# Kernel tuning notes

Measured on AMD Instinct MI355X. Metric: run time of the kernel, lower is better.

Reference implementation:

```python
import jax, jax.numpy as jnp
import numpy as np

N_NODES = 100000
N_EDGES = 3200000
IN_F = 128


def gcn_conv(x, edge_index, edge_weight, W, b):
    """PyG GCNConv: add self-loops (weight 1), symmetric normalization,
    scatter-add aggregation from src -> dst, then bias."""
    n = x.shape[0]
    src, dst = edge_index[0], edge_index[1]
    h = x @ W  # [N, out]
    # degree with self-loop weight 1
    deg = jax.ops.segment_sum(edge_weight, dst, num_segments=n) + 1.0
    dinv = jax.lax.rsqrt(deg)
    norm = dinv[src] * edge_weight * dinv[dst]  # [E]
    msgs = norm[:, None] * h[src]  # [E, out]
    out = jax.ops.segment_sum(msgs, dst, num_segments=n)
    # self-loop contribution: norm = dinv*1*dinv = 1/deg
    out = out + h / deg[:, None]
    return out + b


def setup_inputs() -> dict:
    key = jax.random.key(0)
    ks = jax.random.split(key, 12)
    x = jax.random.normal(ks[0], (N_NODES, IN_F), dtype=jnp.float32)
    edge_index = jax.random.randint(ks[1], (2, N_EDGES), 0, N_NODES)
    edge_weights = jax.random.uniform(ks[2], (N_EDGES,), dtype=jnp.float32)
    def glorot(k, shape):
        lim = np.sqrt(6.0 / (shape[0] + shape[1]))
        return jax.random.uniform(k, shape, jnp.float32, -lim, lim)
    return {
        "x": x,
        "edge_index": edge_index,
        "edge_weights": edge_weights,
        "W1": glorot(ks[3], (IN_F, 32)),
        "b1": jnp.zeros((32,), jnp.float32),
        "W2": glorot(ks[4], (32, 16)),
        "b2": jnp.zeros((16,), jnp.float32),
        "fc1_w": glorot(ks[5], (16, 1)),
        "fc1_b": jnp.zeros((1,), jnp.float32),
        "fc2_w": glorot(ks[6], (33, 1)),
        "fc2_b": jnp.zeros((1,), jnp.float32),
    }


def reference(x, edge_index, edge_weights, W1, b1, W2, b2, fc1_w, fc1_b, fc2_w, fc2_b):
    x1 = gcn_conv(x, edge_index, edge_weights, W1, b1)
    h = jax.nn.relu(x1)  # dropout is identity in eval mode
    x2 = gcn_conv(h, edge_index, edge_weights, W2, b2)
    x1f = x2 @ fc1_w + fc1_b        # [N, 1]
    c = jax.nn.sigmoid(x1f)
    cat = jnp.concatenate([h, c], axis=1)  # [N, 33]
    r = cat @ fc2_w + fc2_b         # [N, 1]
    return (r, x1f)
```

## Files before the change

kernel.cpp:

```cpp
#include <hip/hip_runtime.h>
#include <math.h>


#define TPB 256
#define PA_CHUNK 4096
#define KMAXB 512
#define NPW 8

__global__ __launch_bounds__(512) void countA_kernel(const int* __restrict__ dst,
                                                     int* __restrict__ gtot,
                                                     int E, int K) {
    __shared__ int lhist[KMAXB];
    const int tid = threadIdx.x;
    const int e0  = blockIdx.x * PA_CHUNK;
    if (tid < KMAXB) lhist[tid] = 0;
    __syncthreads();
#pragma unroll
    for (int i = 0; i < 8; ++i) {
        int e = e0 + tid + i * 512;
        if (e < E) atomicAdd(&lhist[dst[e] >> 8], 1);
    }
    __syncthreads();
    if (tid < K && lhist[tid] > 0) atomicAdd(&gtot[tid], lhist[tid]);
}

__global__ __launch_bounds__(64) void kscan_kernel(const int* __restrict__ gtot,
                                                   int* __restrict__ gstart,
                                                   int* __restrict__ gcursor,
                                                   int K, int E) {
    int tid = threadIdx.x;
    int b0 = tid * 8, v[8], s = 0;
#pragma unroll
    for (int t = 0; t < 8; ++t) {
        v[t] = s;
        int idx = b0 + t;
        s += (idx < K) ? gtot[idx] : 0;
    }
    int incl = s;
#pragma unroll
    for (int d = 1; d < 64; d <<= 1) {
        int t2 = __shfl_up(incl, d);
        if (tid >= d) incl += t2;
    }
    int excl = incl - s;
#pragma unroll
    for (int t = 0; t < 8; ++t) {
        int idx = b0 + t;
        if (idx < K) { gstart[idx] = excl + v[t]; gcursor[idx] = excl + v[t]; }
    }
    if (tid == 63) gstart[K] = E;
}

__global__ __launch_bounds__(512) void placeA_kernel(const int* __restrict__ src,
                                                     const int* __restrict__ dst,
                                                     const float* __restrict__ ew,
                                                     uint2* __restrict__ tmp,
                                                     int* __restrict__ gcursor,
                                                     int E, int K) {
    __shared__ int lhist[KMAXB], lbase[KMAXB], lcur[KMAXB], gbaseS[KMAXB];
    __shared__ int ltot;
    __shared__ uint2 stage[PA_CHUNK];
    __shared__ int   saddr[PA_CHUNK];
    const int tid = threadIdx.x;
    const int e0  = blockIdx.x * PA_CHUNK;

    if (tid < KMAXB) { lhist[tid] = 0; lcur[tid] = 0; }
    __syncthreads();

    int   b[8];
    uint2 p[8];
#pragma unroll
    for (int i = 0; i < 8; ++i) {
        int e = e0 + tid + i * 512;
        b[i] = -1;
        if (e < E) {
            int d   = dst[e];
            int s   = src[e];
            float w = ew[e];
            b[i]   = d >> 8;
            p[i].x = __float_as_uint(w);
            p[i].y = ((unsigned)s << 8) | (unsigned)(d & 255);
            atomicAdd(&lhist[b[i]], 1);
        }
    }
    __syncthreads();

    if (tid < 64) {
        int b0 = tid * 8, v[8], s = 0;
#pragma unroll
        for (int t = 0; t < 8; ++t) { v[t] = s; s += lhist[b0 + t]; }
        int incl = s;
#pragma unroll
        for (int d = 1; d < 64; d <<= 1) {
            int t2 = __shfl_up(incl, d);
            if (tid >= d) incl += t2;
        }
        int excl = incl - s;
#pragma unroll
        for (int t = 0; t < 8; ++t) lbase[b0 + t] = excl + v[t];
        if (tid == 63) ltot = incl;
    }
    __syncthreads();

    if (tid < K && lhist[tid] > 0)
        gbaseS[tid] = atomicAdd(&gcursor[tid], lhist[tid]);
    __syncthreads();

#pragma unroll
    for (int i = 0; i < 8; ++i) {
        if (b[i] >= 0) {
            int r    = atomicAdd(&lcur[b[i]], 1);
            int sidx = lbase[b[i]] + r;
            stage[sidx] = p[i];
            saddr[sidx] = gbaseS[b[i]] + r;
        }
    }
    __syncthreads();

    int tot = ltot;
    for (int s = tid; s < tot; s += 512) tmp[saddr[s]] = stage[s];
}

__global__ __launch_bounds__(512) void partB_kernel(const uint2* __restrict__ tmp,
                                                    const int* __restrict__ gstart,
                                                    int2* __restrict__ epair,
                                                    int* __restrict__ off,
                                                    float* __restrict__ dinv,
                                                    int N) {
    __shared__ int   lhist[256], loff[256], lcur[256];
    __shared__ float ldeg[256];
    const int tid  = threadIdx.x;
    const int k    = blockIdx.x;
    const int seg0 = gstart[k], seg1 = gstart[k + 1];

    if (tid < 256) { lhist[tid] = 0; lcur[tid] = 0; ldeg[tid] = 0.f; }
    __syncthreads();

    for (int j = seg0 + tid; j < seg1; j += 512)
        atomicAdd(&lhist[tmp[j].y & 255u], 1);
    __syncthreads();

    if (tid < 64) {
        int b0 = tid * 4, v[4], s = 0;
#pragma unroll
        for (int t = 0; t < 4; ++t) { v[t] = s; s += lhist[b0 + t]; }
        int incl = s;
#pragma unroll
        for (int d = 1; d < 64; d <<= 1) {
            int t2 = __shfl_up(incl, d);
            if (tid >= d) incl += t2;
        }
        int excl = incl - s;
#pragma unroll
        for (int t = 0; t < 4; ++t) loff[b0 + t] = excl + v[t];
    }
    __syncthreads();

    if (tid < 256) {
        int d = (k << 8) + tid;
        if (d < N) off[d] = seg0 + loff[tid];
    }

    for (int j = seg0 + tid; j < seg1; j += 512) {
        uint2 q  = tmp[j];
        int dlow = q.y & 255u;
        int s    = (int)(q.y >> 8);
        float w  = __uint_as_float(q.x);
        int r    = atomicAdd(&lcur[dlow], 1);
        int2 pr; pr.x = s; pr.y = (int)q.x;
        epair[seg0 + loff[dlow] + r] = pr;
        atomicAdd(&ldeg[dlow], w);
    }
    __syncthreads();

    if (tid < 256) {
        int d = (k << 8) + tid;
        if (d < N) dinv[d] = 1.0f / sqrtf(ldeg[tid] + 1.0f);
    }
}

__global__ __launch_bounds__(TPB) void gemm1_kernel(const float* __restrict__ x,
                                                    const float* __restrict__ W,
                                                    const float* __restrict__ dinv,
                                                    float* __restrict__ h, int N) {
    __shared__ float Ws[128 * 32];
    __shared__ float xs[32 * 129];
    const int tid = threadIdx.x;
    const int nb  = blockIdx.x * 32;

    const float4* W4  = (const float4*)W;
    float4*       Ws4 = (float4*)Ws;
#pragma unroll
    for (int i = 0; i < 4; ++i) Ws4[tid + i * 256] = W4[tid + i * 256];

#pragma unroll
    for (int i = 0; i < 4; ++i) {
        int idx  = tid + i * 256;
        int node = idx >> 5;
        int col4 = idx & 31;
        if (nb + node < N) {
            float4 v = ((const float4*)(x + (size_t)nb * 128))[idx];
            float* p = &xs[node * 129 + col4 * 4];
            p[0] = v.x; p[1] = v.y; p[2] = v.z; p[3] = v.w;
        }
    }
    __syncthreads();

    const int nl = tid >> 3;
    const int og = (tid & 7) * 4;
    float a0 = 0.f, a1 = 0.f, a2 = 0.f, a3 = 0.f;
#pragma unroll 8
    for (int k = 0; k < 128; ++k) {
        float xv = xs[nl * 129 + k];
        const float* wp = &Ws[k * 32 + og];
        a0 = fmaf(xv, wp[0], a0);
        a1 = fmaf(xv, wp[1], a1);
        a2 = fmaf(xv, wp[2], a2);
        a3 = fmaf(xv, wp[3], a3);
    }
    int node = nb + nl;
    if (node < N) {
        float dv = dinv[node];
        float* out = &h[(size_t)node * 32 + og];
        out[0] = a0 * dv; out[1] = a1 * dv; out[2] = a2 * dv; out[3] = a3 * dv;
    }
}

__global__ __launch_bounds__(TPB) void gather32_fused_kernel(
    const int* __restrict__ off, const int2* __restrict__ epair,
    const float* __restrict__ g1, const float* __restrict__ dinv,
    const float* __restrict__ b1, const float* __restrict__ W2,
    const float* __restrict__ fc2_w,
    float* __restrict__ g2, float* __restrict__ rdot, int N, int E) {
    __shared__ float wls[544];
    const int tid = threadIdx.x;
    wls[tid]       = W2[tid];
    wls[tid + 256] = W2[tid + 256];
    if (tid < 32) wls[512 + tid] = fc2_w[tid];
    __syncthreads();

    const int lane = tid & 63;
    const int f    = lane & 31;
    const int half = lane >> 5;
    const float bv = b1[f];
    const int wbase = (lane < 16) ? lane : 512;
    const int wstrd = (lane < 16) ? 16 : 1;

    const int i0 = (blockIdx.x * (TPB / 64) + (tid >> 6)) * NPW;

    for (int t = 0; t < NPW; ++t) {
        int i = i0 + t;
        if (i >= N) return;
        const int s0 = off[i];
        const int s1 = (i + 1 < N) ? off[i + 1] : E;

        float acc = 0.f;
        int j = s0 + half;
        for (; j + 6 < s1; j += 8) {
            int2 pa = epair[j];
            int2 pb = epair[j + 2];
            int2 pc = epair[j + 4];
            int2 pd = epair[j + 6];
            acc = fmaf(__int_as_float(pa.y), g1[(size_t)pa.x * 32 + f], acc);
            acc = fmaf(__int_as_float(pb.y), g1[(size_t)pb.x * 32 + f], acc);
            acc = fmaf(__int_as_float(pc.y), g1[(size_t)pc.x * 32 + f], acc);
            acc = fmaf(__int_as_float(pd.y), g1[(size_t)pd.x * 32 + f], acc);
        }
        for (; j < s1; j += 2) {
            int2 p = epair[j];
            acc = fmaf(__int_as_float(p.y), g1[(size_t)p.x * 32 + f], acc);
        }
        acc += __shfl_xor(acc, 32);

        float dv = dinv[i];
        float v  = fmaxf(dv * (acc + g1[(size_t)i * 32 + f]) + bv, 0.f);

        float hs = 0.f;
#pragma unroll
        for (int k = 0; k < 32; ++k)
            hs = fmaf(__shfl(v, k), wls[wbase + k * wstrd], hs);

        if (lane < 16)       g2[(size_t)i * 16 + lane] = hs * dv;
        else if (lane == 16) rdot[i] = hs;
    }
}

__global__ __launch_bounds__(TPB) void gather16_final_kernel(
    const int* __restrict__ off, const int2* __restrict__ epair,
    const float* __restrict__ g2, const float* __restrict__ rdot,
    const float* __restrict__ dinv, const float* __restrict__ b2,
    const float* __restrict__ fc1_w, const float* __restrict__ fc1_b,
    const float* __restrict__ fc2_w, const float* __restrict__ fc2_b,
    float* __restrict__ out, int N, int E) {
    const int tid  = threadIdx.x;
    const int lane = tid & 63;
    const int f    = lane & 15;
    const int q    = lane >> 4;
    const float b2v = b2[f];
    const float f1v = fc1_w[f];
    const float f1b = fc1_b[0];
    const float f2w = fc2_w[32];
    const float f2b = fc2_b[0];

    const int i0 = (blockIdx.x * (TPB / 64) + (tid >> 6)) * NPW;

    for (int t = 0; t < NPW; ++t) {
        int i = i0 + t;
        if (i >= N) return;
        const int s0 = off[i];
        const int s1 = (i + 1 < N) ? off[i + 1] : E;

        float acc = 0.f;
        int j = s0 + q;
        for (; j + 12 < s1; j += 16) {
            int2 pa = epair[j];
            int2 pb = epair[j + 4];
            int2 pc = epair[j + 8];
            int2 pd = epair[j + 12];
            acc = fmaf(__int_as_float(pa.y), g2[(size_t)pa.x * 16 + f], acc);
            acc = fmaf(__int_as_float(pb.y), g2[(size_t)pb.x * 16 + f], acc);
            acc = fmaf(__int_as_float(pc.y), g2[(size_t)pc.x * 16 + f], acc);
            acc = fmaf(__int_as_float(pd.y), g2[(size_t)pd.x * 16 + f], acc);
        }
        for (; j < s1; j += 4) {
            int2 p = epair[j];
            acc = fmaf(__int_as_float(p.y), g2[(size_t)p.x * 16 + f], acc);
        }
        acc += __shfl_xor(acc, 16);
        acc += __shfl_xor(acc, 32);

        float dv = dinv[i];
        float x2 = dv * (acc + g2[(size_t)i * 16 + f]) + b2v;

        float part = x2 * f1v;
        part += __shfl_xor(part, 1);
        part += __shfl_xor(part, 2);
        part += __shfl_xor(part, 4);
        part += __shfl_xor(part, 8);
        float x1f = part + f1b;
        float c   = 1.0f / (1.0f + expf(-x1f));
        float r   = fmaf(c, f2w, f2b) + rdot[i];

        if (lane == 0) {
            out[i]     = r;
            out[N + i] = x1f;
        }
    }
}

extern "C" void kernel_launch(void* const* d_in, const int* in_sizes, int n_in,
                              void* d_out, int out_size, void* d_ws, size_t ws_size,
                              hipStream_t stream) {
    const float* x     = (const float*)d_in[0];
    const int*   ei    = (const int*)d_in[1];
    const float* ew    = (const float*)d_in[2];
    const float* W1    = (const float*)d_in[3];
    const float* b1    = (const float*)d_in[4];
    const float* W2    = (const float*)d_in[5];
    const float* b2    = (const float*)d_in[6];
    const float* fc1_w = (const float*)d_in[7];
    const float* fc1_b = (const float*)d_in[8];
    const float* fc2_w = (const float*)d_in[9];
    const float* fc2_b = (const float*)d_in[10];

    const int N = in_sizes[0] / 128;
    const int E = in_sizes[2];
    const int* src = ei;
    const int* dst = ei + E;
    const int K = (N + 255) >> 8;

    float* ws    = (float*)d_ws;
    float* dinv  = ws;
    float* big   = dinv + N;
    float* g1    = big;
    float* g2    = big + (size_t)32 * N;
    float* rdot  = big + (size_t)48 * N;
    int*   off   = (int*)(big + (size_t)64 * N);
    int2*  epair = (int2*)(off + N);
    int*   gcursor = (int*)(epair + E);
    int*   gstart  = gcursor + K;
    uint2* tmp   = (uint2*)big;

    size_t need = ((size_t)66 * N + (size_t)2 * E + 2 * K + 2) * 4;
    if (ws_size < need || K > KMAXB || (size_t)E > (size_t)32 * N) return;

    hipMemsetAsync(gcursor, 0, (size_t)K * sizeof(int), stream);

    countA_kernel<<<(E + PA_CHUNK - 1) / PA_CHUNK, 512, 0, stream>>>(dst, gcursor, E, K);
    kscan_kernel<<<1, 64, 0, stream>>>(gcursor, gstart, gcursor, K, E);
    placeA_kernel<<<(E + PA_CHUNK - 1) / PA_CHUNK, 512, 0, stream>>>(
        src, dst, ew, tmp, gcursor, E, K);
    partB_kernel<<<K, 512, 0, stream>>>(tmp, gstart, epair, off, dinv, N);

    gemm1_kernel<<<(N + 31) / 32, TPB, 0, stream>>>(x, W1, dinv, g1, N);

    const int gblocks = (N + 4 * NPW - 1) / (4 * NPW);
    gather32_fused_kernel<<<gblocks, TPB, 0, stream>>>(
        off, epair, g1, dinv, b1, W2, fc2_w, g2, rdot, N, E);
    gather16_final_kernel<<<gblocks, TPB, 0, stream>>>(
        off, epair, g2, rdot, dinv, b2, fc1_w, fc1_b, fc2_w, fc2_b,
        (float*)d_out, N, E);
}
```

Baseline: 384.0 us.

## Project layer-2 features onto fc1 before aggregation to gather scalars

Because fc1 is linear, the second GCN aggregation followed by the fc1 projection is reordered: each node's 16-wide g2 row is first dotted with fc1_w into a scalar z, and then only scalars are aggregated over edges. The bias term b2·fc1_w + fc1_b is folded into a constant. This shrinks the per-edge gather in the final kernel from a 16-float row to one float, at the cost of one extra small kernel launch and a change in floating-point summation order.

```diff
diff --git a/kernel.cpp b/kernel.cpp
--- a/kernel.cpp
+++ b/kernel.cpp
@@ -285,20 +285,37 @@
     }
 }
 
-__global__ __launch_bounds__(TPB) void gather16_final_kernel(
+__global__ __launch_bounds__(TPB) void zprep_kernel(const float* __restrict__ g2,
+                                                    const float* __restrict__ fc1_w,
+                                                    float* __restrict__ z, int N) {
+    int i = blockIdx.x * TPB + threadIdx.x;
+    if (i >= N) return;
+    const float4* g4 = (const float4*)(g2 + (size_t)i * 16);
+    float acc = 0.f;
+#pragma unroll
+    for (int q = 0; q < 4; ++q) {
+        float4 v = g4[q];
+        acc = fmaf(v.x, fc1_w[q * 4 + 0], acc);
+        acc = fmaf(v.y, fc1_w[q * 4 + 1], acc);
+        acc = fmaf(v.z, fc1_w[q * 4 + 2], acc);
+        acc = fmaf(v.w, fc1_w[q * 4 + 3], acc);
+    }
+    z[i] = acc;
+}
+
+__global__ __launch_bounds__(TPB) void final_scalar_kernel(
     const int* __restrict__ off, const int2* __restrict__ epair,
-    const float* __restrict__ g2, const float* __restrict__ rdot,
+    const float* __restrict__ z, const float* __restrict__ rdot,
     const float* __restrict__ dinv, const float* __restrict__ b2,
     const float* __restrict__ fc1_w, const float* __restrict__ fc1_b,
     const float* __restrict__ fc2_w, const float* __restrict__ fc2_b,
     float* __restrict__ out, int N, int E) {
     const int tid  = threadIdx.x;
     const int lane = tid & 63;
-    const int f    = lane & 15;
-    const int q    = lane >> 4;
-    const float b2v = b2[f];
-    const float f1v = fc1_w[f];
-    const float f1b = fc1_b[0];
+
+    float C = fc1_b[0];
+#pragma unroll
+    for (int f = 0; f < 16; ++f) C = fmaf(b2[f], fc1_w[f], C);
     const float f2w = fc2_w[32];
     const float f2b = fc2_b[0];
 
@@ -311,33 +328,18 @@
         const int s1 = (i + 1 < N) ? off[i + 1] : E;
 
         float acc = 0.f;
-        int j = s0 + q;
-        for (; j + 12 < s1; j += 16) {
-            int2 pa = epair[j];
-            int2 pb = epair[j + 4];
-            int2 pc = epair[j + 8];
-            int2 pd = epair[j + 12];
-            acc = fmaf(__int_as_float(pa.y), g2[(size_t)pa.x * 16 + f], acc);
-            acc = fmaf(__int_as_float(pb.y), g2[(size_t)pb.x * 16 + f], acc);
-            acc = fmaf(__int_as_float(pc.y), g2[(size_t)pc.x * 16 + f], acc);
-            acc = fmaf(__int_as_float(pd.y), g2[(size_t)pd.x * 16 + f], acc);
-        }
-        for (; j < s1; j += 4) {
+        for (int j = s0 + lane; j < s1; j += 64) {
             int2 p = epair[j];
-            acc = fmaf(__int_as_float(p.y), g2[(size_t)p.x * 16 + f], acc);
-        }
+            acc = fmaf(__int_as_float(p.y), z[p.x], acc);
+        }
+        acc += __shfl_xor(acc, 1);
+        acc += __shfl_xor(acc, 2);
+        acc += __shfl_xor(acc, 4);
+        acc += __shfl_xor(acc, 8);
         acc += __shfl_xor(acc, 16);
         acc += __shfl_xor(acc, 32);
 
-        float dv = dinv[i];
-        float x2 = dv * (acc + g2[(size_t)i * 16 + f]) + b2v;
-
-        float part = x2 * f1v;
-        part += __shfl_xor(part, 1);
-        part += __shfl_xor(part, 2);
-        part += __shfl_xor(part, 4);
-        part += __shfl_xor(part, 8);
-        float x1f = part + f1b;
+        float x1f = dinv[i] * (acc + z[i]) + C;
         float c   = 1.0f / (1.0f + expf(-x1f));
         float r   = fmaf(c, f2w, f2b) + rdot[i];
 
@@ -375,6 +377,7 @@
     float* g1    = big;
     float* g2    = big + (size_t)32 * N;
     float* rdot  = big + (size_t)48 * N;
+    float* z     = big + (size_t)49 * N;
     int*   off   = (int*)(big + (size_t)64 * N);
     int2*  epair = (int2*)(off + N);
     int*   gcursor = (int*)(epair + E);
@@ -397,7 +400,8 @@
     const int gblocks = (N + 4 * NPW - 1) / (4 * NPW);
     gather32_fused_kernel<<<gblocks, TPB, 0, stream>>>(
         off, epair, g1, dinv, b1, W2, fc2_w, g2, rdot, N, E);
-    gather16_final_kernel<<<gblocks, TPB, 0, stream>>>(
-        off, epair, g2, rdot, dinv, b2, fc1_w, fc1_b, fc2_w, fc2_b,
+    zprep_kernel<<<(N + TPB - 1) / TPB, TPB, 0, stream>>>(g2, fc1_w, z, N);
+    final_scalar_kernel<<<gblocks, TPB, 0, stream>>>(
+        off, epair, z, rdot, dinv, b2, fc1_w, fc1_b, fc2_w, fc2_b,
         (float*)d_out, N, E);
 }
```

New measurement: 345.1 us. -10.1%, faster.
